# Kernel optimization log

Measured on AMD Instinct MI355X. Metric: run time of the kernel, lower is better.

The kernel has to match this reference:

```python
import jax, jax.numpy as jnp
import numpy as np

B, IN, OUT, N, K = 2048, 4096, 4096, 64, 4  # batch, in_features, out_features, num_nodes, degree


def setup_inputs() -> dict:
    key = jax.random.key(0)
    k0, k1, k2, k3 = jax.random.split(key, 4)
    x = jax.random.normal(k0, (B, IN), dtype=jnp.float32)
    # kaiming-ish init for the linear weight
    W = jax.random.normal(k1, (OUT, IN), dtype=jnp.float32) * (1.0 / np.sqrt(IN))
    ecoeff = jax.random.uniform(k2, (N, N), dtype=jnp.float32, minval=0.1, maxval=0.5)
    phase = jax.random.uniform(k3, (N, N), dtype=jnp.float32, minval=0.0, maxval=2.0 * np.pi)
    tension = jnp.ones((N,), dtype=jnp.float32)
    # deterministic degree-K ring topology: paths[i] = [(i+1..i+K) % N]
    src = jnp.repeat(jnp.arange(N), K).astype(jnp.int32)            # [E]
    dst = ((src + jnp.tile(jnp.arange(1, K + 1), N)) % N).astype(jnp.int32)  # [E]
    return {"x": x, "W": W, "ecoeff": ecoeff, "phase": phase,
            "tension": tension, "src": src, "dst": dst}


def reference(x, W, ecoeff, phase, tension, src, dst):
    # EntangledConnectionLayer.forward
    b = x.shape[0]
    out_features = W.shape[0]
    n = tension.shape[0]
    opn = out_features // n  # out_per_node

    out = x @ W.T  # [B, OUT] == F.linear(x, weights)
    nodes = out.reshape(b, n, opn)  # [B, N, opn] node-sliced view of output

    # entangled_connection_function on a real signal:
    # real(sig * (1 + eps*exp(i*phi)) / (1 + tau_i*tau_j)) = sig*(1+eps*cos(phi))/(1+tau_i*tau_j)
    eps = ecoeff[src, dst]                    # [E]
    phi = phase[src, dst]                     # [E]
    tau = tension[src] * tension[dst]         # [E]
    scale = (1.0 + eps * jnp.cos(phi)) / (1.0 + tau)  # [E]

    contrib = nodes[:, src, :] * scale[None, :, None]  # [B, E, opn]
    entangled = jnp.zeros_like(nodes).at[:, dst, :].add(contrib)  # scatter-add over edges

    return out + 0.5 * entangled.reshape(b, out_features)
```

## Files before the change

kernel.cpp:

```cpp
#include <hip/hip_runtime.h>
#include <hip/hip_bf16.h>

#define TILE 128
#define BK   64
#define BKG  128

typedef __attribute__((ext_vector_type(8))) short bf16x8;
typedef __attribute__((ext_vector_type(4))) float f32x4;

__device__ __forceinline__ unsigned short f32_to_bf16(float f) {
    unsigned u = __float_as_uint(f);
    unsigned rounded = u + 0x7FFF + ((u >> 16) & 1);
    return (unsigned short)(rounded >> 16);
}
__device__ __forceinline__ float bf16_to_f32(unsigned short h) {
    return __uint_as_float(((unsigned)h) << 16);
}
__device__ __forceinline__ bool probe_f32(const void* tens) {
    return ((const unsigned short*)tens)[0] == 0;
}

__global__ __launch_bounds__(256)
void prep_kernel(const void* __restrict__ xv, const void* __restrict__ Wv,
                 const void* __restrict__ ecoeff, const void* __restrict__ phase,
                 const void* __restrict__ tens,
                 const int* __restrict__ srcIdx, const int* __restrict__ dstIdx,
                 unsigned short* __restrict__ xa, unsigned short* __restrict__ wp,
                 int E, int K, int castB)
{
    constexpr int NODES = 64, CHUNK = 256, CAP = 8;
    __shared__ unsigned short buf[NODES * CHUNK];
    __shared__ int   cnt[NODES];
    __shared__ int   slist[NODES * CAP];
    __shared__ float clist[NODES * CAP];

    const bool isF32 = probe_f32(tens);
    const int tid = threadIdx.x;
    const int b   = blockIdx.x;

    if (b < castB) {
        const size_t i = ((size_t)b * 256 + tid) * 8;
        if (isF32) {
            const float4 a = *(const float4*)((const float*)xv + i);
            const float4 c = *(const float4*)((const float*)xv + i + 4);
            unsigned short p[8];
            p[0]=f32_to_bf16(a.x); p[1]=f32_to_bf16(a.y); p[2]=f32_to_bf16(a.z); p[3]=f32_to_bf16(a.w);
            p[4]=f32_to_bf16(c.x); p[5]=f32_to_bf16(c.y); p[6]=f32_to_bf16(c.z); p[7]=f32_to_bf16(c.w);
            *(bf16x8*)(xa + i) = *(const bf16x8*)p;
        } else {
            *(bf16x8*)(xa + i) = *(const bf16x8*)((const unsigned short*)xv + i);
        }
        return;
    }

    const int wb = b - castB;
    const int j  = wb & 63;
    const int k0 = (wb >> 6) * CHUNK;

    if (tid < NODES) cnt[tid] = 0;
    __syncthreads();
    if (tid < E) {
        const int s = srcIdx[tid];
        const int d = dstIdx[tid];
        float eps, phi, ts, td;
        if (isF32) {
            eps = ((const float*)ecoeff)[s * NODES + d];
            phi = ((const float*)phase)[s * NODES + d];
            ts  = ((const float*)tens)[s];
            td  = ((const float*)tens)[d];
        } else {
            eps = bf16_to_f32(((const unsigned short*)ecoeff)[s * NODES + d]);
            phi = bf16_to_f32(((const unsigned short*)phase)[s * NODES + d]);
            ts  = bf16_to_f32(((const unsigned short*)tens)[s]);
            td  = bf16_to_f32(((const unsigned short*)tens)[d]);
        }
        const float coef = 0.5f * (1.0f + eps * __cosf(phi)) / (1.0f + ts * td);
        const int pos = atomicAdd(&cnt[d], 1);
        if (pos < CAP) { slist[d * CAP + pos] = s; clist[d * CAP + pos] = coef; }
    }

    if (isF32) {
        for (int idx = tid; idx < NODES * CHUNK / 4; idx += 256) {
            const int s = idx >> 6;
            const int p = idx & 63;
            const float4 v = *(const float4*)
                ((const float*)Wv + (size_t)(s * 64 + j) * K + k0 + p * 4);
            ushort4 u;
            u.x = f32_to_bf16(v.x); u.y = f32_to_bf16(v.y);
            u.z = f32_to_bf16(v.z); u.w = f32_to_bf16(v.w);
            *(ushort4*)&buf[s * CHUNK + p * 4] = u;
        }
    } else {
        for (int idx = tid; idx < NODES * CHUNK / 4; idx += 256) {
            const int s = idx >> 6;
            const int p = idx & 63;
            *(ushort4*)&buf[s * CHUNK + p * 4] = *(const ushort4*)
                ((const unsigned short*)Wv + (size_t)(s * 64 + j) * K + k0 + p * 4);
        }
    }
    __syncthreads();

    const int kk4  = (tid & 63) * 4;
    const int dgrp = (tid >> 6) * 16;
#pragma unroll 4
    for (int dd = 0; dd < 16; ++dd) {
        const int d = dgrp + dd;
        const ushort4 a = *(const ushort4*)&buf[d * CHUNK + kk4];
        float v0 = bf16_to_f32(a.x), v1 = bf16_to_f32(a.y);
        float v2 = bf16_to_f32(a.z), v3 = bf16_to_f32(a.w);
        const int n = cnt[d] < CAP ? cnt[d] : CAP;
        for (int t = 0; t < n; ++t) {
            const float c = clist[d * CAP + t];
            const ushort4 s4 = *(const ushort4*)&buf[slist[d * CAP + t] * CHUNK + kk4];
            v0 += c * bf16_to_f32(s4.x); v1 += c * bf16_to_f32(s4.y);
            v2 += c * bf16_to_f32(s4.z); v3 += c * bf16_to_f32(s4.w);
        }
        ushort4 o;
        o.x = f32_to_bf16(v0); o.y = f32_to_bf16(v1);
        o.z = f32_to_bf16(v2); o.w = f32_to_bf16(v3);
        *(ushort4*)(wp + (size_t)(d * 64 + j) * K + k0 + kk4) = o;
    }
}

__global__ __launch_bounds__(256)
void gemm_ws_kernel(const unsigned short* __restrict__ A,
                    const unsigned short* __restrict__ B,
                    void* __restrict__ Cv, const void* __restrict__ tens,
                    int M, int N, int K)
{
    __shared__ __align__(16) unsigned short As[TILE * BKG];
    __shared__ __align__(16) unsigned short Bs[TILE * BKG];

    const bool isF32 = probe_f32(tens);
    const int tid  = threadIdx.x;
    const int lane = tid & 63;
    const int w    = tid >> 6;
    const int wm   = (w >> 1) * 64;
    const int wn   = (w & 1) * 64;
    const int m0   = blockIdx.y * TILE;
    const int n0   = blockIdx.x * TILE;

    f32x4 acc[4][4] = {};

    const int lrow   = lane >> 4;
    const int lchunk = lane & 15;

    for (int k0 = 0; k0 < K; k0 += BKG) {
#pragma unroll
        for (int t = 0; t < 8; ++t) {
            const int br  = t * 16 + w * 4;
            const int row = br + lrow;
            const int gsw = ((lchunk & 7) ^ (row & 7)) | (lchunk & 8);
            const unsigned short* ga = A + (size_t)(m0 + row) * K + (k0 + gsw * 8);
            const unsigned short* gb = B + (size_t)(n0 + row) * K + (k0 + gsw * 8);
            __builtin_amdgcn_global_load_lds(
                (__attribute__((address_space(1))) const void*)ga,
                (__attribute__((address_space(3))) void*)&As[br * BKG], 16, 0, 0);
            __builtin_amdgcn_global_load_lds(
                (__attribute__((address_space(1))) const void*)gb,
                (__attribute__((address_space(3))) void*)&Bs[br * BKG], 16, 0, 0);
        }
        __syncthreads();

#pragma unroll
        for (int kk = 0; kk < BKG; kk += 32) {
            const int rr = lane & 15;
            const int c  = (kk >> 3) + (lane >> 4);
            const int slot = (((c & 7) ^ (rr & 7)) | (c & 8)) * 8;
            bf16x8 av[4], bv[4];
#pragma unroll
            for (int i = 0; i < 4; ++i)
                av[i] = *(const bf16x8*)&As[(wm + i * 16 + rr) * BKG + slot];
#pragma unroll
            for (int i = 0; i < 4; ++i)
                bv[i] = *(const bf16x8*)&Bs[(wn + i * 16 + rr) * BKG + slot];
#pragma unroll
            for (int mt = 0; mt < 4; ++mt)
#pragma unroll
                for (int nt = 0; nt < 4; ++nt)
                    acc[mt][nt] = __builtin_amdgcn_mfma_f32_16x16x32_bf16(
                        av[mt], bv[nt], acc[mt][nt], 0, 0, 0);
        }
        __syncthreads();
    }

    const int quad = (lane >> 4) * 4;
    const int col  = lane & 15;
#pragma unroll
    for (int mt = 0; mt < 4; ++mt)
#pragma unroll
        for (int nt = 0; nt < 4; ++nt)
#pragma unroll
            for (int r = 0; r < 4; ++r) {
                const size_t gr = (size_t)(m0 + wm + mt * 16 + quad + r);
                const size_t gc = (size_t)(n0 + wn + nt * 16 + col);
                const float v = acc[mt][nt][r];
                if (isF32) ((float*)Cv)[gr * N + gc] = v;
                else       ((unsigned short*)Cv)[gr * N + gc] = f32_to_bf16(v);
            }
}

__global__ __launch_bounds__(256)
void gemm_bt_kernel(const void* __restrict__ Av, const void* __restrict__ Bv,
                    void* __restrict__ Cv, const void* __restrict__ tens,
                    int M, int N, int K)
{
    __shared__ __align__(16) short As[TILE * BK];
    __shared__ __align__(16) short Bs[TILE * BK];

    const bool isF32 = probe_f32(tens);
    const int tid  = threadIdx.x;
    const int lane = tid & 63;
    const int w    = tid >> 6;
    const int wm   = (w >> 1) * 64;
    const int wn   = (w & 1) * 64;
    const int m0   = blockIdx.y * TILE;
    const int n0   = blockIdx.x * TILE;
    f32x4 acc[4][4] = {};
    const int lrow = lane >> 3;
    const int lcol = (lane & 7) * 8;

    for (int k0 = 0; k0 < K; k0 += BK) {
        if (!isF32) {
            const short* A = (const short*)Av;
            const short* B = (const short*)Bv;
#pragma unroll
            for (int t = 0; t < 4; ++t) {
                const int br = t * 32 + w * 8;
                const short* ga = A + (size_t)(m0 + br + lrow) * K + (k0 + lcol);
                const short* gb = B + (size_t)(n0 + br + lrow) * K + (k0 + lcol);
                __builtin_amdgcn_global_load_lds(
                    (__attribute__((address_space(1))) const void*)ga,
                    (__attribute__((address_space(3))) void*)&As[br * BK], 16, 0, 0);
                __builtin_amdgcn_global_load_lds(
                    (__attribute__((address_space(1))) const void*)gb,
                    (__attribute__((address_space(3))) void*)&Bs[br * BK], 16, 0, 0);
            }
        } else {
            const float* A = (const float*)Av;
            const float* B = (const float*)Bv;
#pragma unroll
            for (int t = 0; t < 4; ++t) {
                const int br = t * 32 + w * 8;
                const int row = br + lrow;
                const float* ga = A + (size_t)(m0 + row) * K + (k0 + lcol);
                const float* gb = B + (size_t)(n0 + row) * K + (k0 + lcol);
                float4 a0 = *(const float4*)(ga);
                float4 a1 = *(const float4*)(ga + 4);
                float4 b0 = *(const float4*)(gb);
                float4 b1 = *(const float4*)(gb + 4);
                short pa[8], pb[8];
                pa[0]=f32_to_bf16(a0.x); pa[1]=f32_to_bf16(a0.y);
                pa[2]=f32_to_bf16(a0.z); pa[3]=f32_to_bf16(a0.w);
                pa[4]=f32_to_bf16(a1.x); pa[5]=f32_to_bf16(a1.y);
                pa[6]=f32_to_bf16(a1.z); pa[7]=f32_to_bf16(a1.w);
                pb[0]=f32_to_bf16(b0.x); pb[1]=f32_to_bf16(b0.y);
                pb[2]=f32_to_bf16(b0.z); pb[3]=f32_to_bf16(b0.w);
                pb[4]=f32_to_bf16(b1.x); pb[5]=f32_to_bf16(b1.y);
                pb[6]=f32_to_bf16(b1.z); pb[7]=f32_to_bf16(b1.w);
                *(bf16x8*)&As[row * BK + lcol] = *(const bf16x8*)pa;
                *(bf16x8*)&Bs[row * BK + lcol] = *(const bf16x8*)pb;
            }
        }
        __syncthreads();
#pragma unroll
        for (int kk = 0; kk < BK; kk += 32) {
            const int rk = kk + (lane >> 4) * 8;
            const int rr = lane & 15;
            bf16x8 av[4], bv[4];
#pragma unroll
            for (int i = 0; i < 4; ++i)
                av[i] = *(const bf16x8*)&As[(wm + i * 16 + rr) * BK + rk];
#pragma unroll
            for (int i = 0; i < 4; ++i)
                bv[i] = *(const bf16x8*)&Bs[(wn + i * 16 + rr) * BK + rk];
#pragma unroll
            for (int mt = 0; mt < 4; ++mt)
#pragma unroll
                for (int nt = 0; nt < 4; ++nt)
                    acc[mt][nt] = __builtin_amdgcn_mfma_f32_16x16x32_bf16(
                        av[mt], bv[nt], acc[mt][nt], 0, 0, 0);
        }
        __syncthreads();
    }
    const int quad = (lane >> 4) * 4;
    const int col  = lane & 15;
#pragma unroll
    for (int mt = 0; mt < 4; ++mt)
#pragma unroll
        for (int nt = 0; nt < 4; ++nt)
#pragma unroll
            for (int r = 0; r < 4; ++r) {
                const size_t gr = (size_t)(m0 + wm + mt * 16 + quad + r);
                const size_t gc = (size_t)(n0 + wn + nt * 16 + col);
                const float v = acc[mt][nt][r];
                if (isF32) ((float*)Cv)[gr * N + gc] = v;
                else       ((unsigned short*)Cv)[gr * N + gc] = f32_to_bf16(v);
            }
}

__global__ __launch_bounds__(256)
void entangle_kernel(void* __restrict__ Cv,
                     const void* __restrict__ ecoeff,
                     const void* __restrict__ phase,
                     const void* __restrict__ tens,
                     const int* __restrict__ srcIdx,
                     const int* __restrict__ dstIdx,
                     int E)
{
    constexpr int NODES = 64, OPN = 64, FEAT = 4096, ROWS = 2, CAP = 8;
    __shared__ float rows[ROWS * FEAT];
    __shared__ int   cnt[NODES];
    __shared__ int   slist[NODES * CAP];
    __shared__ float clist[NODES * CAP];

    const bool isF32 = probe_f32(tens);
    const int tid = threadIdx.x;
    if (tid < NODES) cnt[tid] = 0;
    __syncthreads();

    if (tid < E) {
        const int s = srcIdx[tid];
        const int d = dstIdx[tid];
        float eps, phi, ts, td;
        if (isF32) {
            eps = ((const float*)ecoeff)[s * NODES + d];
            phi = ((const float*)phase)[s * NODES + d];
            ts  = ((const float*)tens)[s];
            td  = ((const float*)tens)[d];
        } else {
            eps = bf16_to_f32(((const unsigned short*)ecoeff)[s * NODES + d]);
            phi = bf16_to_f32(((const unsigned short*)phase)[s * NODES + d]);
            ts  = bf16_to_f32(((const unsigned short*)tens)[s]);
            td  = bf16_to_f32(((const unsigned short*)tens)[d]);
        }
        const float coef = 0.5f * (1.0f + eps * __cosf(phi)) / (1.0f + ts * td);
        const int pos = atomicAdd(&cnt[d], 1);
        if (pos < CAP) { slist[d * CAP + pos] = s; clist[d * CAP + pos] = coef; }
    }

    const size_t row0 = (size_t)blockIdx.x * ROWS;
    if (isF32) {
        const float4* g = (const float4*)((const float*)Cv + row0 * FEAT);
        float4* l = (float4*)rows;
        for (int i = tid; i < ROWS * FEAT / 4; i += 256) l[i] = g[i];
    } else {
        const ushort2* g = (const ushort2*)((const unsigned short*)Cv + row0 * FEAT);
        for (int i = tid; i < ROWS * FEAT / 2; i += 256) {
            const ushort2 u = g[i];
            rows[i * 2 + 0] = bf16_to_f32(u.x);
            rows[i * 2 + 1] = bf16_to_f32(u.y);
        }
    }
    __syncthreads();

    for (int c = 0; c < ROWS * FEAT / 256; ++c) {
        const int i = c * 256 + tid;
        const int r = i >> 12;
        const int o = i & (FEAT - 1);
        const int d = o >> 6;
        const int j = o & (OPN - 1);
        float v = rows[i];
        const int n = cnt[d] < CAP ? cnt[d] : CAP;
        for (int t = 0; t < n; ++t)
            v += clist[d * CAP + t] * rows[(r << 12) + slist[d * CAP + t] * OPN + j];
        if (isF32) ((float*)Cv)[(row0 + r) * FEAT + o] = v;
        else       ((unsigned short*)Cv)[(row0 + r) * FEAT + o] = f32_to_bf16(v);
    }
}

extern "C" void kernel_launch(void* const* d_in, const int* in_sizes, int n_in,
                              void* d_out, int out_size, void* d_ws, size_t ws_size,
                              hipStream_t stream)
{
    const void* x       = d_in[0];
    const void* W       = d_in[1];
    const void* ecoeff  = d_in[2];
    const void* phase   = d_in[3];
    const void* tension = d_in[4];
    const int*  src     = (const int*)d_in[5];
    const int*  dst     = (const int*)d_in[6];

    const int INF  = 4096;
    const int OUTF = 4096;
    const int M    = in_sizes[0] / INF;
    const int E    = in_sizes[5];

    const size_t needA = (size_t)M * INF * sizeof(unsigned short);
    const size_t needW = (size_t)OUTF * INF * sizeof(unsigned short);

    if (ws_size >= needA + needW) {
        unsigned short* xa = (unsigned short*)d_ws;
        unsigned short* wp = (unsigned short*)((char*)d_ws + needA);

        const int castB = (M * INF) / (256 * 8);
        const int wpB   = 64 * (INF / 256);
        prep_kernel<<<dim3(castB + wpB), dim3(256), 0, stream>>>(
            x, W, ecoeff, phase, tension, src, dst, xa, wp, E, INF, castB);
        gemm_ws_kernel<<<dim3(OUTF / TILE, M / TILE), dim3(256), 0, stream>>>(
            xa, wp, d_out, tension, M, OUTF, INF);
    } else {
        dim3 grid(OUTF / TILE, M / TILE), block(256);
        gemm_bt_kernel<<<grid, block, 0, stream>>>(x, W, d_out, tension, M, OUTF, INF);
        entangle_kernel<<<dim3(M / 2), block, 0, stream>>>(
            d_out, ecoeff, phase, tension, src, dst, E);
    }
}
```

Before: 221.5 us.

## Replace GEMM with 8-wave 128x256 triple-buffered pipelined kernel

Replaces the single-buffered 128x128 bf16 GEMM with a 512-thread kernel on 128x256 tiles and BK=64, triple-buffered in LDS. Global-to-LDS prefetches for tile t+2 are split into two phases and interleaved with the MFMA phases, using explicit vmcnt/lgkmcnt waits, barriers and s_setprio. The aim is to hide memory latency behind compute and remove the full sync stall after each K step. In exchange the kernel uses more LDS and registers per block and depends on hand-tuned wait counts for correctness.

New measurement: 221.9 us. Within noise of the previous version (+0.2%).

```diff
diff --git a/kernel.cpp b/kernel.cpp
--- a/kernel.cpp
+++ b/kernel.cpp
@@ -3,7 +3,10 @@
 
 #define TILE 128
 #define BK   64
-#define BKG  128
+
+#define BM8 128
+#define BN8 256
+#define BK8 64
 
 typedef __attribute__((ext_vector_type(8))) short bf16x8;
 typedef __attribute__((ext_vector_type(4))) float f32x4;
@@ -122,66 +125,120 @@
     }
 }
 
-__global__ __launch_bounds__(256)
-void gemm_ws_kernel(const unsigned short* __restrict__ A,
-                    const unsigned short* __restrict__ B,
-                    void* __restrict__ Cv, const void* __restrict__ tens,
-                    int M, int N, int K)
+#define GLOAD(g, l) __builtin_amdgcn_global_load_lds( \
+        (__attribute__((address_space(1))) const void*)(g), \
+        (__attribute__((address_space(3))) void*)(l), 16, 0, 0)
+
+__global__ __launch_bounds__(512)
+void gemm8_kernel(const unsigned short* __restrict__ A,
+                  const unsigned short* __restrict__ B,
+                  void* __restrict__ Cv, const void* __restrict__ tens,
+                  int M, int N, int K)
 {
-    __shared__ __align__(16) unsigned short As[TILE * BKG];
-    __shared__ __align__(16) unsigned short Bs[TILE * BKG];
+    __shared__ __align__(16) unsigned short As[3][BM8 * BK8];
+    __shared__ __align__(16) unsigned short Bs[3][BN8 * BK8];
 
     const bool isF32 = probe_f32(tens);
+    asm volatile("" :: "v"((int)isF32));
+
     const int tid  = threadIdx.x;
     const int lane = tid & 63;
     const int w    = tid >> 6;
-    const int wm   = (w >> 1) * 64;
-    const int wn   = (w & 1) * 64;
-    const int m0   = blockIdx.y * TILE;
-    const int n0   = blockIdx.x * TILE;
+    const int wm   = (w >> 2) * 64;
+    const int wn   = (w & 3) * 64;
+    const int m0   = blockIdx.y * BM8;
+    const int n0   = blockIdx.x * BN8;
+
+    const int rsub = lane >> 3;
+    const int csw  = ((lane & 7) ^ rsub) * 8;
+    const int arow0 = w * 16;
+    const int brow0 = w * 32;
+
+    const unsigned short* aSrc = A + (size_t)(m0 + arow0 + rsub) * K + csw;
+    const unsigned short* bSrc = B + (size_t)(n0 + brow0 + rsub) * K + csw;
+
+    const int rr  = lane & 15;
+    const int kq  = lane >> 4;
+    const int sw7 = rr & 7;
+    const int sl0 = (kq ^ sw7) * 8;
+    const int sl1 = ((4 + kq) ^ sw7) * 8;
 
     f32x4 acc[4][4] = {};
 
-    const int lrow   = lane >> 4;
-    const int lchunk = lane & 15;
-
-    for (int k0 = 0; k0 < K; k0 += BKG) {
-#pragma unroll
-        for (int t = 0; t < 8; ++t) {
-            const int br  = t * 16 + w * 4;
-            const int row = br + lrow;
-            const int gsw = ((lchunk & 7) ^ (row & 7)) | (lchunk & 8);
-            const unsigned short* ga = A + (size_t)(m0 + row) * K + (k0 + gsw * 8);
-            const unsigned short* gb = B + (size_t)(n0 + row) * K + (k0 + gsw * 8);
-            __builtin_amdgcn_global_load_lds(
-                (__attribute__((address_space(1))) const void*)ga,
-                (__attribute__((address_space(3))) void*)&As[br * BKG], 16, 0, 0);
-            __builtin_amdgcn_global_load_lds(
-                (__attribute__((address_space(1))) const void*)gb,
-                (__attribute__((address_space(3))) void*)&Bs[br * BKG], 16, 0, 0);
-        }
-        __syncthreads();
-
-#pragma unroll
-        for (int kk = 0; kk < BKG; kk += 32) {
-            const int rr = lane & 15;
-            const int c  = (kk >> 3) + (lane >> 4);
-            const int slot = (((c & 7) ^ (rr & 7)) | (c & 8)) * 8;
-            bf16x8 av[4], bv[4];
-#pragma unroll
-            for (int i = 0; i < 4; ++i)
-                av[i] = *(const bf16x8*)&As[(wm + i * 16 + rr) * BKG + slot];
-#pragma unroll
-            for (int i = 0; i < 4; ++i)
-                bv[i] = *(const bf16x8*)&Bs[(wn + i * 16 + rr) * BKG + slot];
-#pragma unroll
-            for (int mt = 0; mt < 4; ++mt)
-#pragma unroll
-                for (int nt = 0; nt < 4; ++nt)
-                    acc[mt][nt] = __builtin_amdgcn_mfma_f32_16x16x32_bf16(
-                        av[mt], bv[nt], acc[mt][nt], 0, 0, 0);
-        }
-        __syncthreads();
+    const int NT = K / BK8;
+
+#define STAGE_P0(kt, bi) do { \
+        const unsigned short* as_ = aSrc + (size_t)(kt) * BK8; \
+        const unsigned short* bs_ = bSrc + (size_t)(kt) * BK8; \
+        GLOAD(as_,                  &As[bi][(arow0     ) * BK8]); \
+        GLOAD(as_ + (size_t)8 * K,  &As[bi][(arow0 +  8) * BK8]); \
+        GLOAD(bs_,                  &Bs[bi][(brow0     ) * BK8]); \
+    } while (0)
+#define STAGE_P1(kt, bi) do { \
+        const unsigned short* bs_ = bSrc + (size_t)(kt) * BK8; \
+        GLOAD(bs_ + (size_t)8  * K, &Bs[bi][(brow0 +  8) * BK8]); \
+        GLOAD(bs_ + (size_t)16 * K, &Bs[bi][(brow0 + 16) * BK8]); \
+        GLOAD(bs_ + (size_t)24 * K, &Bs[bi][(brow0 + 24) * BK8]); \
+    } while (0)
+
+    STAGE_P0(0, 0); STAGE_P1(0, 0);
+    STAGE_P0(1, 1); STAGE_P1(1, 1);
+    asm volatile("s_waitcnt vmcnt(6)" ::: "memory");
+    __builtin_amdgcn_s_barrier();
+    __builtin_amdgcn_sched_barrier(0);
+
+    int cur = 0;
+    for (int t = 0; t < NT; ++t) {
+        int nb = cur + 2; if (nb >= 3) nb -= 3;
+        const bool pf = (t + 2 < NT);
+        const unsigned short* asC = &As[cur][0];
+        const unsigned short* bsC = &Bs[cur][0];
+
+        bf16x8 av0[4], bv0[4];
+#pragma unroll
+        for (int i = 0; i < 4; ++i)
+            av0[i] = *(const bf16x8*)&asC[(wm + i * 16 + rr) * BK8 + sl0];
+#pragma unroll
+        for (int i = 0; i < 4; ++i)
+            bv0[i] = *(const bf16x8*)&bsC[(wn + i * 16 + rr) * BK8 + sl0];
+        if (pf) STAGE_P0(t + 2, nb);
+        __builtin_amdgcn_s_barrier();
+        asm volatile("s_waitcnt lgkmcnt(0)");
+        __builtin_amdgcn_s_setprio(1);
+#pragma unroll
+        for (int mt = 0; mt < 4; ++mt)
+#pragma unroll
+            for (int nc = 0; nc < 4; ++nc)
+                acc[mt][nc] = __builtin_amdgcn_mfma_f32_16x16x32_bf16(
+                    av0[mt], bv0[nc], acc[mt][nc], 0, 0, 0);
+        __builtin_amdgcn_s_setprio(0);
+        __builtin_amdgcn_s_barrier();
+
+        bf16x8 av1[4], bv1[4];
+#pragma unroll
+        for (int i = 0; i < 4; ++i)
+            av1[i] = *(const bf16x8*)&asC[(wm + i * 16 + rr) * BK8 + sl1];
+#pragma unroll
+        for (int i = 0; i < 4; ++i)
+            bv1[i] = *(const bf16x8*)&bsC[(wn + i * 16 + rr) * BK8 + sl1];
+        if (pf) STAGE_P1(t + 2, nb);
+        __builtin_amdgcn_s_barrier();
+        asm volatile("s_waitcnt lgkmcnt(0)");
+        __builtin_amdgcn_s_setprio(1);
+#pragma unroll
+        for (int mt = 0; mt < 4; ++mt)
+#pragma unroll
+            for (int nc = 0; nc < 4; ++nc)
+                acc[mt][nc] = __builtin_amdgcn_mfma_f32_16x16x32_bf16(
+                    av1[mt], bv1[nc], acc[mt][nc], 0, 0, 0);
+        __builtin_amdgcn_s_setprio(0);
+
+        if (pf)                 asm volatile("s_waitcnt vmcnt(6)" ::: "memory");
+        else if (t + 1 < NT)    asm volatile("s_waitcnt vmcnt(0)" ::: "memory");
+        __builtin_amdgcn_s_barrier();
+        __builtin_amdgcn_sched_barrier(0);
+
+        cur = cur + 1; if (cur == 3) cur = 0;
     }
 
     const int quad = (lane >> 4) * 4;
@@ -189,12 +246,12 @@
 #pragma unroll
     for (int mt = 0; mt < 4; ++mt)
 #pragma unroll
-        for (int nt = 0; nt < 4; ++nt)
+        for (int nc = 0; nc < 4; ++nc)
 #pragma unroll
             for (int r = 0; r < 4; ++r) {
                 const size_t gr = (size_t)(m0 + wm + mt * 16 + quad + r);
-                const size_t gc = (size_t)(n0 + wn + nt * 16 + col);
-                const float v = acc[mt][nt][r];
+                const size_t gc = (size_t)(n0 + wn + nc * 16 + col);
+                const float v = acc[mt][nc][r];
                 if (isF32) ((float*)Cv)[gr * N + gc] = v;
                 else       ((unsigned short*)Cv)[gr * N + gc] = f32_to_bf16(v);
             }
@@ -389,7 +446,7 @@
     const size_t needA = (size_t)M * INF * sizeof(unsigned short);
     const size_t needW = (size_t)OUTF * INF * sizeof(unsigned short);
 
-    if (ws_size >= needA + needW) {
+    if (ws_size >= needA + needW && (M % BM8) == 0) {
         unsigned short* xa = (unsigned short*)d_ws;
         unsigned short* wp = (unsigned short*)((char*)d_ws + needA);
 
@@ -397,7 +454,7 @@
         const int wpB   = 64 * (INF / 256);
         prep_kernel<<<dim3(castB + wpB), dim3(256), 0, stream>>>(
             x, W, ecoeff, phase, tension, src, dst, xa, wp, E, INF, castB);
-        gemm_ws_kernel<<<dim3(OUTF / TILE, M / TILE), dim3(256), 0, stream>>>(
+        gemm8_kernel<<<dim3(OUTF / BN8, M / BM8), dim3(512), 0, stream>>>(
             xa, wp, d_out, tension, M, OUTF, INF);
     } else {
         dim3 grid(OUTF / TILE, M / TILE), block(256);
```
